# Optimization experiments

Measured on AMD Instinct MI355X. Metric: run time of the kernel, lower is better.

The kernel has to match this reference:

```python
import jax, jax.numpy as jnp
import numpy as np

B, IN, O, F, FH = 512, 2000, 64, 8, 32
D = 64 + FH * O  # 2112


def setup_inputs() -> dict:
    key = jax.random.key(0)
    ks = jax.random.split(key, 17)
    rn = lambda k, s: jax.random.normal(k, s, dtype=jnp.float32) * 0.05
    return dict(
        x=rn(ks[0], (B, IN)),
        fc_in_W=rn(ks[1], (1024, IN)), fc_in_b=rn(ks[2], (1024,)),
        fc1_W=rn(ks[3], (128, 1024)), fc1_b=rn(ks[4], (128,)),
        out1_W=rn(ks[5], (O, 64, 128)), out1_b=rn(ks[6], (O, 64)),
        coef_nn_W=rn(ks[7], (F, FH, 1)), coef_nn_b=rn(ks[8], (F, FH)),
        coef_att_W=rn(ks[9], (F, FH, FH)),
        out_att_W=rn(ks[10], (O, FH, FH)),
        nodes_trans_W=rn(ks[11], (O, O)),
        trans_gcn_W=rn(ks[12], (D, D)),
        outmap_W=rn(ks[13], (1, D)), outmap_b=rn(ks[14], (1,)),
        prelu_a=jnp.float32(0.25),
        coef_m=rn(ks[15], (O, O, F)),
    )


def reference(x, fc_in_W, fc_in_b, fc1_W, fc1_b, out1_W, out1_b,
              coef_nn_W, coef_nn_b, coef_att_W, out_att_W,
              nodes_trans_W, trans_gcn_W, outmap_W, outmap_b, prelu_a, coef_m):
    elu = jax.nn.elu
    # trunk MLP
    h = jax.nn.relu(x @ fc_in_W.T + fc_in_b)          # [B,1024]
    h = jax.nn.relu(h @ fc1_W.T + fc1_b)              # [B,128]
    # per-output-node heads (vectorized over the output_dim loop)
    hiddens = jax.nn.relu(jnp.einsum('bk,odk->bod', h, out1_W) + out1_b)  # [B,O,64]
    # per-feature coef embedding: Linear(1,FH) on each coef_m[:,:,i] slice
    cf = elu(coef_m[..., None] * coef_nn_W[:, :, 0] + coef_nn_b)          # [O,O,F,FH]
    # sum over concatenated feature axis (F*FH) of exp(elu(.))
    s = jnp.exp(elu(cf)).sum(axis=(2, 3))[:, :, None, None]               # [O,O,1,1]
    lin = jnp.einsum('xyfh,fgh->xyfg', cf, coef_att_W)                    # per-feature attention linear
    p = elu(jnp.exp(elu(cf)) * lin / s)
    cfs = elu(p.sum(axis=2) / F)                                          # [O,O,FH]
    # node-level attention (vectorized over the output_dim loop)
    coef_sum = jnp.exp(elu(cfs)).sum(axis=1)                              # [O,FH]
    p2 = jnp.exp(elu(cfs)) / coef_sum[:, None, :]                         # [O,O,FH]
    lin2 = jnp.einsum('oih,igh->oig', cfs, out_att_W)
    att = (p2 * lin2).reshape(O, O * FH)                                  # concat over i (i-major)
    hc = jnp.concatenate(
        [hiddens, jnp.broadcast_to(att[None], (x.shape[0], O, O * FH))], axis=2)  # [B,O,D]
    nt = jnp.einsum('bpd,op->bod', hc, nodes_trans_W)                     # node mixing Linear(O,O)
    trans = jax.nn.sigmoid(jnp.einsum('bod,ed->boe', nt, trans_gcn_W))    # [B,O,D]
    z = (trans @ outmap_W.T + outmap_b).squeeze(-1)                       # [B,O]
    return jnp.where(z >= 0, z, prelu_a * z)                              # PReLU
```

## Files before the change

### kernel.cpp

```cpp
#include <hip/hip_runtime.h>
#include <math.h>

typedef __attribute__((ext_vector_type(8))) short bf16x8;
typedef __attribute__((ext_vector_type(4))) float f32x4;

static __device__ __forceinline__ float fast_elu(float x) {
    return x > 0.0f ? x : __expf(x) - 1.0f;
}

static __device__ __forceinline__ unsigned short f2bf(float f) {
    unsigned int u = __float_as_uint(f);
    unsigned int r = (u + 0x7FFFu + ((u >> 16) & 1u)) >> 16;
    return (unsigned short)r;
}

static __device__ __forceinline__ bf16x8 cvt8(const float* __restrict__ s) {
    float4 a = *reinterpret_cast<const float4*>(s);
    float4 b = *reinterpret_cast<const float4*>(s + 4);
    bf16x8 r;
    r[0] = (short)f2bf(a.x); r[1] = (short)f2bf(a.y);
    r[2] = (short)f2bf(a.z); r[3] = (short)f2bf(a.w);
    r[4] = (short)f2bf(b.x); r[5] = (short)f2bf(b.y);
    r[6] = (short)f2bf(b.z); r[7] = (short)f2bf(b.w);
    return r;
}

#define S0 131072
#define S1 393216
#define S2 409600
#define S3 410112
#define S4 475648
#define S5 492544
#define CONV_BLOCKS 1924

static __device__ __forceinline__ void conv_phase(
    int bx,
    const float* __restrict__ x, const float* __restrict__ fcinW,
    const float* __restrict__ fc1W, const float* __restrict__ ntW,
    const float* __restrict__ out1W, const float* __restrict__ tgw,
    unsigned short* __restrict__ xb, unsigned short* __restrict__ fcinWb,
    unsigned short* __restrict__ fc1Wb, unsigned short* __restrict__ Wb,
    unsigned short* __restrict__ out1WbT, unsigned short* __restrict__ Gb)
{
    int u = bx * 256 + threadIdx.x;
    if (u < S0) {
        int r = u >> 8, c = u & 255;
        bf16x8 v;
        if (c < 250) v = cvt8(&x[(size_t)r * 2000 + c * 8]);
        else { bf16x8 z = {0,0,0,0,0,0,0,0}; v = z; }
        *reinterpret_cast<bf16x8*>(&xb[(size_t)r * 2048 + c * 8]) = v;
    } else if (u < S1) {
        int i = u - S0;
        int r = i >> 8, c = i & 255;
        bf16x8 v;
        if (c < 250) v = cvt8(&fcinW[(size_t)r * 2000 + c * 8]);
        else { bf16x8 z = {0,0,0,0,0,0,0,0}; v = z; }
        *reinterpret_cast<bf16x8*>(&fcinWb[(size_t)r * 2048 + c * 8]) = v;
    } else if (u < S2) {
        int i8 = (u - S1) * 8;
        *reinterpret_cast<bf16x8*>(&fc1Wb[i8]) = cvt8(&fc1W[i8]);
    } else if (u < S3) {
        int i8 = (u - S2) * 8;
        *reinterpret_cast<bf16x8*>(&Wb[i8]) = cvt8(&ntW[i8]);
    } else if (u < S4) {
        int i = u - S3;
        int n = i >> 4, kc = i & 15;
        int d = n >> 6, p = n & 63;
        *reinterpret_cast<bf16x8*>(&out1WbT[(size_t)n * 128 + kc * 8]) =
            cvt8(&out1W[(size_t)((p << 6) | d) * 128 + kc * 8]);
    } else if (u < S5) {
        int i = u - S4;
        int e = i >> 3, c = i & 7;
        *reinterpret_cast<bf16x8*>(&Gb[(size_t)e * 64 + c * 8]) =
            cvt8(&tgw[(size_t)e * 2112 + c * 8]);
    }
}

static __device__ __forceinline__ void coef_phase(
    int bx, float* __restrict__ smemf,
    const float* __restrict__ coef_m, const float* __restrict__ cW,
    const float* __restrict__ cB, const float* __restrict__ attW,
    float* __restrict__ cfs)
{
    float* cf_s = smemf;
    float* part = smemf + 1024;
    const int t = threadIdx.x;
    const int wv = t >> 6, lane = t & 63;
    const int xy = bx * 4 + wv;
    float ls = 0.0f;
    #pragma unroll
    for (int i = 0; i < 4; ++i) {
        int idx = i * 64 + lane;
        int f = idx >> 5;
        float v = fast_elu(coef_m[xy * 8 + f] * cW[idx] + cB[idx]);
        cf_s[wv * 256 + idx] = v;
        ls += __expf(fast_elu(v));
    }
    #pragma unroll
    for (int m = 1; m < 64; m <<= 1) ls += __shfl_xor(ls, m, 64);
    __syncthreads();
    const float rs = __builtin_amdgcn_rcpf(ls);
    const int g = lane & 31, fg = lane >> 5;
    float acc = 0.0f;
    for (int f = fg * 4; f < fg * 4 + 4; ++f) {
        float lin = 0.0f;
        #pragma unroll
        for (int h = 0; h < 32; h += 4) {
            float4 Lv = *reinterpret_cast<const float4*>(&cf_s[wv * 256 + f * 32 + h]);
            float4 Wv = *reinterpret_cast<const float4*>(&attW[f * 1024 + g * 32 + h]);
            lin += Lv.x * Wv.x + Lv.y * Wv.y + Lv.z * Wv.z + Lv.w * Wv.w;
        }
        float e = __expf(fast_elu(cf_s[wv * 256 + f * 32 + g]));
        acc += fast_elu(e * lin * rs);
    }
    part[wv * 64 + lane] = acc;
    __syncthreads();
    if (lane < 32) {
        float tot = part[wv * 64 + lane] + part[wv * 64 + lane + 32];
        cfs[xy * 32 + lane] = fast_elu(tot * 0.125f);
    }
}

static __device__ __forceinline__ void att_phase(
    int o, int ic, float* __restrict__ smemf,
    const float* __restrict__ cfs, const float* __restrict__ oattW,
    float* __restrict__ att)
{
    float* L    = smemf;
    float* red  = smemf + 2048;
    float* csum = smemf + 2304;
    const int t = threadIdx.x;
    #pragma unroll
    for (int j = 0; j < 8; ++j) L[t + 256 * j] = cfs[o * 2048 + t + 256 * j];
    __syncthreads();
    {
        int h = t & 31, ig = t >> 5;
        float ps = 0.0f;
        for (int i = ig * 8; i < ig * 8 + 8; ++i) ps += __expf(fast_elu(L[i * 32 + h]));
        red[t] = ps;
        __syncthreads();
        if (t < 32) {
            float cs = 0.0f;
            #pragma unroll
            for (int j = 0; j < 8; ++j) cs += red[j * 32 + t];
            csum[t] = cs;
        }
        __syncthreads();
    }
    int idx = ic * 256 + t;
    int i = idx >> 5, g = idx & 31;
    float lin2 = 0.0f;
    #pragma unroll
    for (int h = 0; h < 32; h += 4) {
        float4 Lv = *reinterpret_cast<const float4*>(&L[i * 32 + h]);
        float4 Wv = *reinterpret_cast<const float4*>(&oattW[i * 1024 + g * 32 + h]);
        lin2 += Lv.x * Wv.x + Lv.y * Wv.y + Lv.z * Wv.z + Lv.w * Wv.w;
    }
    float p2 = __expf(fast_elu(L[idx])) * __builtin_amdgcn_rcpf(csum[g]);
    att[o * 2048 + idx] = p2 * lin2;
}

static __device__ __forceinline__ void natt_phase(
    int bx, float* __restrict__ smemf,
    const float* __restrict__ ntW, const float* __restrict__ att,
    unsigned short* __restrict__ nattb)
{
    float* ntW_s = smemf;
    float* att_s = smemf + 64 * 65;
    const int t = threadIdx.x;
    const int d0 = bx * 16;
    #pragma unroll
    for (int j = 0; j < 16; ++j) {
        int idx = t + 256 * j;
        ntW_s[(idx >> 6) * 65 + (idx & 63)] = ntW[idx];
    }
    #pragma unroll
    for (int j = 0; j < 4; ++j) {
        int idx = t + 256 * j;
        int p = idx >> 4, dd = idx & 15;
        att_s[p * 17 + dd] = att[p * 2048 + d0 + dd];
    }
    __syncthreads();
    const int dd = t & 15, ob = (t >> 4) * 4;
    float acc[4] = {0.0f, 0.0f, 0.0f, 0.0f};
    for (int p = 0; p < 64; ++p) {
        float av = att_s[p * 17 + dd];
        #pragma unroll
        for (int i = 0; i < 4; ++i) acc[i] += ntW_s[(ob + i) * 65 + p] * av;
    }
    #pragma unroll
    for (int i = 0; i < 4; ++i)
        nattb[(ob + i) * 2048 + d0 + dd] = f2bf(acc[i]);
}

static __device__ __forceinline__ void gemm_core(
    const unsigned short* __restrict__ A, int lda,
    const unsigned short* __restrict__ B, int ldb,
    float* __restrict__ C, unsigned short* __restrict__ Cb,
    int ldc, long strideCz, const float* __restrict__ bias,
    int mode, int kchunk, int bn, int bm, int bz,
    unsigned short* __restrict__ As, unsigned short* __restrict__ Bs)
{
    const int t = threadIdx.x;
    const int w = t >> 6, lane = t & 63, l16 = lane & 15, quad = lane >> 4;
    const int n0 = bn * 64, m0 = bm * 64;
    const int kb0 = bz * kchunk;
    const int r = t >> 2, koff = (t & 3) * 8;
    if (mode == 0) C += (size_t)bz * strideCz;

    const size_t arow = (size_t)(m0 + r) * lda + koff;
    const size_t brow = (size_t)(n0 + r) * ldb + koff;
    bf16x8 av = *reinterpret_cast<const bf16x8*>(&A[arow + kb0]);
    bf16x8 bv = *reinterpret_cast<const bf16x8*>(&B[brow + kb0]);

    f32x4 acc[4] = {};
    for (int kb = kb0; kb < kb0 + kchunk; kb += 32) {
        __syncthreads();
        *reinterpret_cast<bf16x8*>(&As[r * 40 + koff]) = av;
        *reinterpret_cast<bf16x8*>(&Bs[r * 40 + koff]) = bv;
        if (kb + 32 < kb0 + kchunk) {
            av = *reinterpret_cast<const bf16x8*>(&A[arow + kb + 32]);
            bv = *reinterpret_cast<const bf16x8*>(&B[brow + kb + 32]);
        }
        __syncthreads();
        bf16x8 af = *reinterpret_cast<const bf16x8*>(&As[(w * 16 + l16) * 40 + quad * 8]);
        #pragma unroll
        for (int nt = 0; nt < 4; ++nt) {
            bf16x8 bf = *reinterpret_cast<const bf16x8*>(&Bs[(nt * 16 + l16) * 40 + quad * 8]);
            acc[nt] = __builtin_amdgcn_mfma_f32_16x16x32_bf16(af, bf, acc[nt], 0, 0, 0);
        }
    }
    #pragma unroll
    for (int nt = 0; nt < 4; ++nt)
        #pragma unroll
        for (int i = 0; i < 4; ++i) {
            int m = m0 + w * 16 + quad * 4 + i;
            int n = n0 + nt * 16 + l16;
            if (mode == 0) {
                C[(size_t)m * ldc + n] = acc[nt][i];
            } else {
                int bidx = (((n & 63) << 6) | (n >> 6));
                float v = acc[nt][i] + bias[bidx];
                v = fmaxf(v, 0.0f);
                Cb[(size_t)m * ldc + n] = f2bf(v);
            }
        }
}

static __device__ __forceinline__ void gemm_tgwa_core(
    const float* __restrict__ tgw,
    const unsigned short* __restrict__ B,
    float* __restrict__ C, long strideCz,
    int kchunk, int bm, int bz,
    unsigned short* __restrict__ As, unsigned short* __restrict__ Bs)
{
    const int t = threadIdx.x;
    const int w = t >> 6, lane = t & 63, l16 = lane & 15, quad = lane >> 4;
    const int m0 = bm * 64;
    const int kb0 = bz * kchunk;
    const int r = t >> 2, koff = (t & 3) * 8;
    C += (size_t)bz * strideCz;

    const float* arow = tgw + (size_t)(m0 + r) * 2112 + 64 + koff;
    const unsigned short* brow = B + (size_t)r * 2048 + koff;
    bf16x8 av = cvt8(arow + kb0);
    bf16x8 bv = *reinterpret_cast<const bf16x8*>(brow + kb0);

    f32x4 acc[4] = {};
    for (int kb = kb0; kb < kb0 + kchunk; kb += 32) {
        __syncthreads();
        *reinterpret_cast<bf16x8*>(&As[r * 40 + koff]) = av;
        *reinterpret_cast<bf16x8*>(&Bs[r * 40 + koff]) = bv;
        if (kb + 32 < kb0 + kchunk) {
            av = cvt8(arow + kb + 32);
            bv = *reinterpret_cast<const bf16x8*>(brow + kb + 32);
        }
        __syncthreads();
        bf16x8 af = *reinterpret_cast<const bf16x8*>(&As[(w * 16 + l16) * 40 + quad * 8]);
        #pragma unroll
        for (int nt = 0; nt < 4; ++nt) {
            bf16x8 bf = *reinterpret_cast<const bf16x8*>(&Bs[(nt * 16 + l16) * 40 + quad * 8]);
            acc[nt] = __builtin_amdgcn_mfma_f32_16x16x32_bf16(af, bf, acc[nt], 0, 0, 0);
        }
    }
    #pragma unroll
    for (int nt = 0; nt < 4; ++nt)
        #pragma unroll
        for (int i = 0; i < 4; ++i) {
            int m = m0 + w * 16 + quad * 4 + i;
            int n = nt * 16 + l16;
            C[(size_t)m * 64 + n] = acc[nt][i];
        }
}

static __device__ __forceinline__ void gemm_fa_core(
    const float* __restrict__ Ap, int lda, long apstride, int nparts,
    const float* __restrict__ abias,
    const unsigned short* __restrict__ B, int ldb,
    float* __restrict__ C, unsigned short* __restrict__ Cb,
    int ldc, long strideCz, const float* __restrict__ bias,
    int mode, int kchunk, int bn, int bm, int bz,
    unsigned short* __restrict__ As, unsigned short* __restrict__ Bs)
{
    const int t = threadIdx.x;
    const int w = t >> 6, lane = t & 63, l16 = lane & 15, quad = lane >> 4;
    const int n0 = bn * 64, m0 = bm * 64;
    const int kb0 = bz * kchunk;
    const int r = t >> 2, koff = (t & 3) * 8;
    if (mode == 0) C += (size_t)bz * strideCz;

    f32x4 acc[4] = {};
    for (int kb = kb0; kb < kb0 + kchunk; kb += 32) {
        float a8[8];
        {
            const float* base = &Ap[(size_t)(m0 + r) * lda + kb + koff];
            float4 s0 = *reinterpret_cast<const float4*>(base);
            float4 s1 = *reinterpret_cast<const float4*>(base + 4);
            for (int j = 1; j < nparts; ++j) {
                const float* pj = base + (size_t)j * apstride;
                float4 p0 = *reinterpret_cast<const float4*>(pj);
                float4 p1 = *reinterpret_cast<const float4*>(pj + 4);
                s0.x += p0.x; s0.y += p0.y; s0.z += p0.z; s0.w += p0.w;
                s1.x += p1.x; s1.y += p1.y; s1.z += p1.z; s1.w += p1.w;
            }
            float4 b0 = *reinterpret_cast<const float4*>(&abias[kb + koff]);
            float4 b1 = *reinterpret_cast<const float4*>(&abias[kb + koff + 4]);
            a8[0] = fmaxf(s0.x + b0.x, 0.0f); a8[1] = fmaxf(s0.y + b0.y, 0.0f);
            a8[2] = fmaxf(s0.z + b0.z, 0.0f); a8[3] = fmaxf(s0.w + b0.w, 0.0f);
            a8[4] = fmaxf(s1.x + b1.x, 0.0f); a8[5] = fmaxf(s1.y + b1.y, 0.0f);
            a8[6] = fmaxf(s1.z + b1.z, 0.0f); a8[7] = fmaxf(s1.w + b1.w, 0.0f);
        }
        bf16x8 bv = *reinterpret_cast<const bf16x8*>(&B[(size_t)(n0 + r) * ldb + kb + koff]);
        __syncthreads();
        ushort4 lo, hi;
        lo.x = f2bf(a8[0]); lo.y = f2bf(a8[1]); lo.z = f2bf(a8[2]); lo.w = f2bf(a8[3]);
        hi.x = f2bf(a8[4]); hi.y = f2bf(a8[5]); hi.z = f2bf(a8[6]); hi.w = f2bf(a8[7]);
        *reinterpret_cast<ushort4*>(&As[r * 40 + koff]) = lo;
        *reinterpret_cast<ushort4*>(&As[r * 40 + koff + 4]) = hi;
        *reinterpret_cast<bf16x8*>(&Bs[r * 40 + koff]) = bv;
        __syncthreads();
        bf16x8 af = *reinterpret_cast<const bf16x8*>(&As[(w * 16 + l16) * 40 + quad * 8]);
        #pragma unroll
        for (int nt = 0; nt < 4; ++nt) {
            bf16x8 bf = *reinterpret_cast<const bf16x8*>(&Bs[(nt * 16 + l16) * 40 + quad * 8]);
            acc[nt] = __builtin_amdgcn_mfma_f32_16x16x32_bf16(af, bf, acc[nt], 0, 0, 0);
        }
    }
    #pragma unroll
    for (int nt = 0; nt < 4; ++nt)
        #pragma unroll
        for (int i = 0; i < 4; ++i) {
            int m = m0 + w * 16 + quad * 4 + i;
            int n = n0 + nt * 16 + l16;
            if (mode == 0) {
                C[(size_t)m * ldc + n] = acc[nt][i];
            } else {
                int bidx = (((n & 63) << 6) | (n >> 6));
                float v = acc[nt][i] + bias[bidx];
                v = fmaxf(v, 0.0f);
                Cb[(size_t)m * ldc + n] = f2bf(v);
            }
        }
}

static __device__ __forceinline__ void nt1f_phase(
    int b, unsigned short* __restrict__ smemu,
    const unsigned short* __restrict__ hbT, const unsigned short* __restrict__ Wb,
    unsigned short* __restrict__ nt1b)
{
    unsigned short* HtT   = smemu;
    unsigned short* nt1_s = smemu + 64 * 72;
    const int t = threadIdx.x;
    const int w = t >> 6, lane = t & 63, l16 = lane & 15, quad = lane >> 4;

    const unsigned short* src = hbT + (size_t)b * 4096;
    #pragma unroll
    for (int j = 0; j < 2; ++j) {
        int c = t + j * 256;
        *reinterpret_cast<bf16x8*>(&HtT[(c >> 3) * 72 + (c & 7) * 8]) =
            *reinterpret_cast<const bf16x8*>(&src[c * 8]);
    }
    __syncthreads();

    bf16x8 aW[2];
    #pragma unroll
    for (int h = 0; h < 2; ++h)
        aW[h] = *reinterpret_cast<const bf16x8*>(&Wb[(w * 16 + l16) * 64 + h * 32 + quad * 8]);
    #pragma unroll
    for (int dt = 0; dt < 4; ++dt) {
        f32x4 acc = {0.0f, 0.0f, 0.0f, 0.0f};
        #pragma unroll
        for (int h = 0; h < 2; ++h) {
            bf16x8 bf = *reinterpret_cast<const bf16x8*>(
                &HtT[(dt * 16 + l16) * 72 + h * 32 + quad * 8]);
            acc = __builtin_amdgcn_mfma_f32_16x16x32_bf16(aW[h], bf, acc, 0, 0, 0);
        }
        #pragma unroll
        for (int i = 0; i < 4; ++i)
            nt1_s[(w * 16 + quad * 4 + i) * 72 + dt * 16 + l16] = f2bf(acc[i]);
    }
    __syncthreads();
    #pragma unroll
    for (int j = 0; j < 2; ++j) {
        int c = t + j * 256;
        *reinterpret_cast<bf16x8*>(&nt1b[(size_t)b * 4096 + c * 8]) =
            *reinterpret_cast<const bf16x8*>(&nt1_s[(c >> 3) * 72 + (c & 7) * 8]);
    }
}

__global__ __launch_bounds__(256) void uber1(
    const float* x, const float* fcinW, const float* fc1W, const float* ntW,
    const float* out1W, const float* tgw,
    unsigned short* xb, unsigned short* fcinWb, unsigned short* fc1Wb,
    unsigned short* Wb, unsigned short* out1WbT, unsigned short* Gb,
    const float* coef_m, const float* cW, const float* cB, const float* attW,
    float* cfs)
{
    __shared__ __align__(16) float smemf[1280];
    int bx = blockIdx.x;
    if (bx < CONV_BLOCKS)
        conv_phase(bx, x, fcinW, fc1W, ntW, out1W, tgw,
                   xb, fcinWb, fc1Wb, Wb, out1WbT, Gb);
    else
        coef_phase(bx - CONV_BLOCKS, smemf, coef_m, cW, cB, attW, cfs);
}

__global__ __launch_bounds__(256) void uber2(
    const unsigned short* xb, const unsigned short* fcinWb, float* h1p,
    const float* cfs, const float* oattW, float* att)
{
    __shared__ __align__(16) float smemf[2592];
    int bx = blockIdx.x;
    if (bx < 512) {
        unsigned short* As = (unsigned short*)smemf;
        gemm_core(xb, 2048, fcinWb, 2048, h1p, nullptr, 1024, 524288L,
                  nullptr, 0, 512, bx & 15, (bx >> 4) & 7, bx >> 7, As, As + 2560);
    } else {
        int b2 = bx - 512;
        att_phase(b2 & 63, b2 >> 6, smemf, cfs, oattW, att);
    }
}

__global__ __launch_bounds__(256) void uber3(
    const float* h1p, const float* fc_in_b, const unsigned short* fc1Wb,
    float* h2p,
    const float* ntW, const float* att, unsigned short* nattb)
{
    __shared__ __align__(16) float smemf[5248];
    int bx = blockIdx.x;
    if (bx < 64) {
        unsigned short* As = (unsigned short*)smemf;
        gemm_fa_core(h1p, 1024, 524288L, 4, fc_in_b, fc1Wb, 1024,
                     h2p, nullptr, 128, 65536L, nullptr, 0, 256,
                     bx & 1, (bx >> 1) & 7, bx >> 4, As, As + 2560);
    } else {
        natt_phase(bx - 64, smemf, ntW, att, nattb);
    }
}

__global__ __launch_bounds__(256) void uber4(
    const float* h2p, const float* fc1_b, const unsigned short* out1WbT,
    unsigned short* hbT, const float* out1_b,
    const float* tgw, const unsigned short* nattb, float* cpT)
{
    __shared__ __align__(16) float smemf[2560];
    unsigned short* As = (unsigned short*)smemf;
    int bx = blockIdx.x;
    if (bx < 512) {
        gemm_fa_core(h2p, 128, 65536L, 4, fc1_b, out1WbT, 128,
                     nullptr, hbT, 4096, 0L, out1_b, 2, 128,
                     bx & 63, bx >> 6, 0, As, As + 2560);
    } else {
        int b2 = bx - 512;
        gemm_tgwa_core(tgw, nattb, cpT, 135168L, 256,
                       b2 % 33, b2 / 33, As, As + 2560);
    }
}

__global__ __launch_bounds__(256) void uber5(
    const unsigned short* hbT, const unsigned short* Wb, unsigned short* nt1b,
    const float* cpT, float* cmatT)
{
    __shared__ __align__(16) unsigned short smemu[2 * 64 * 72];
    int bx = blockIdx.x;
    if (bx < 512) {
        nt1f_phase(bx, smemu, hbT, Wb, nt1b);
    } else {
        int i = (bx - 512) * 256 + threadIdx.x;
        if (i < 135168) {
            float a = 0.0f;
            #pragma unroll
            for (int j = 0; j < 8; ++j) a += cpT[i + (long)j * 135168L];
            cmatT[i] = a;
        }
    }
}

__global__ __launch_bounds__(256) void final_nb(
    const unsigned short* __restrict__ nt1b,
    const unsigned short* __restrict__ Gb,
    const float* __restrict__ cmatT,
    const float* __restrict__ outW,
    float* __restrict__ zpart)
{
    const int t = threadIdx.x;
    const int w = t >> 6, lane = t & 63, l16 = lane & 15, quad = lane >> 4;
    const int eb = blockIdx.x;
    const int b0 = blockIdx.y * 16;
    const int o = w * 16 + l16;

    bf16x8 ga[4][2];
    float cm[4][4], wv[4][4];
    #pragma unroll
    for (int et = 0; et < 4; ++et) {
        #pragma unroll
        for (int h = 0; h < 2; ++h)
            ga[et][h] = *reinterpret_cast<const bf16x8*>(
                &Gb[(size_t)(eb * 64 + et * 16 + l16) * 64 + h * 32 + quad * 8]);
        #pragma unroll
        for (int i = 0; i < 4; ++i) {
            int e = eb * 64 + et * 16 + quad * 4 + i;
            cm[et][i] = cmatT[(size_t)e * 64 + o];
            wv[et][i] = outW[e];
        }
    }

    const unsigned short* bbase = nt1b + (size_t)b0 * 4096 + o * 64 + quad * 8;
    bf16x8 bf0 = *reinterpret_cast<const bf16x8*>(bbase);
    bf16x8 bf1 = *reinterpret_cast<const bf16x8*>(bbase + 32);

    for (int bi = 0; bi < 16; ++bi) {
        bf16x8 nb0, nb1;
        if (bi < 15) {
            nb0 = *reinterpret_cast<const bf16x8*>(bbase + (size_t)(bi + 1) * 4096);
            nb1 = *reinterpret_cast<const bf16x8*>(bbase + (size_t)(bi + 1) * 4096 + 32);
        }
        float zo = 0.0f;
        #pragma unroll
        for (int et = 0; et < 4; ++et) {
            f32x4 acc = {cm[et][0], cm[et][1], cm[et][2], cm[et][3]};
            acc = __builtin_amdgcn_mfma_f32_16x16x32_bf16(ga[et][0], bf0, acc, 0, 0, 0);
            acc = __builtin_amdgcn_mfma_f32_16x16x32_bf16(ga[et][1], bf1, acc, 0, 0, 0);
            #pragma unroll
            for (int i = 0; i < 4; ++i)
                zo += __builtin_amdgcn_rcpf(1.0f + __expf(-acc[i])) * wv[et][i];
        }
        zo += __shfl_xor(zo, 16, 64);
        zo += __shfl_xor(zo, 32, 64);
        if (quad == 0)
            zpart[((size_t)eb * 512 + b0 + bi) * 64 + o] = zo;
        bf0 = nb0; bf1 = nb1;
    }
}

__global__ __launch_bounds__(256) void finish_kernel(
    const float* __restrict__ zpart, const float* __restrict__ outB,
    const float* __restrict__ preluA, float* __restrict__ out)
{
    int i = blockIdx.x * 256 + threadIdx.x;
    float z = 0.0f;
    for (int j = 0; j < 33; ++j) z += zpart[(size_t)j * 32768 + i];
    z += outB[0];
    float pa = preluA[0];
    out[i] = (z >= 0.0f) ? z : pa * z;
}

extern "C" void kernel_launch(void* const* d_in, const int* in_sizes, int n_in,
                              void* d_out, int out_size, void* d_ws, size_t ws_size,
                              hipStream_t stream)
{
    const float* x       = (const float*)d_in[0];
    const float* fc_in_W = (const float*)d_in[1];
    const float* fc_in_b = (const float*)d_in[2];
    const float* fc1_W   = (const float*)d_in[3];
    const float* fc1_b   = (const float*)d_in[4];
    const float* out1_W  = (const float*)d_in[5];
    const float* out1_b  = (const float*)d_in[6];
    const float* cW      = (const float*)d_in[7];
    const float* cB      = (const float*)d_in[8];
    const float* cattW   = (const float*)d_in[9];
    const float* oattW   = (const float*)d_in[10];
    const float* ntW     = (const float*)d_in[11];
    const float* tgw     = (const float*)d_in[12];
    const float* outW    = (const float*)d_in[13];
    const float* outB    = (const float*)d_in[14];
    const float* preluA  = (const float*)d_in[15];
    const float* coef_m  = (const float*)d_in[16];
    float* out = (float*)d_out;
    float* ws  = (float*)d_ws;

    unsigned short* xb      = (unsigned short*)(ws + 0);
    unsigned short* fcinWb  = (unsigned short*)(ws + 524288);
    unsigned short* fc1Wb   = (unsigned short*)(ws + 1572864);
    unsigned short* Wb      = (unsigned short*)(ws + 1638400);
    unsigned short* out1WbT = (unsigned short*)(ws + 1640448);
    unsigned short* Gb      = (unsigned short*)(ws + 1902592);
    float*          cfs     = ws + 1970176;
    float*          att     = ws + 2101248;
    unsigned short* nattb   = (unsigned short*)(ws + 2232320);
    float*          h1p     = ws + 2297856;
    float*          h2p     = ws + 4395008;
    unsigned short* hbT     = (unsigned short*)(ws + 4657152);
    float*          cpT     = ws + 5705728;
    float*          cmatT   = ws + 6787072;
    unsigned short* nt1b    = (unsigned short*)(ws + 6922240);
    float*          zpart   = ws + 7970816;

    uber1<<<CONV_BLOCKS + 1024, 256, 0, stream>>>(
        x, fc_in_W, fc1_W, ntW, out1_W, tgw,
        xb, fcinWb, fc1Wb, Wb, out1WbT, Gb,
        coef_m, cW, cB, cattW, cfs);
    uber2<<<1024, 256, 0, stream>>>(xb, fcinWb, h1p, cfs, oattW, att);
    uber3<<<192, 256, 0, stream>>>(h1p, fc_in_b, fc1Wb, h2p, ntW, att, nattb);
    uber4<<<776, 256, 0, stream>>>(h2p, fc1_b, out1WbT, hbT, out1_b,
                                   tgw, nattb, cpT);
    uber5<<<1040, 256, 0, stream>>>(hbT, Wb, nt1b, cpT, cmatT);
    final_nb<<<dim3(33, 32), 256, 0, stream>>>(nt1b, Gb, cmatT, outW, zpart);
    finish_kernel<<<128, 256, 0, stream>>>(zpart, outB, preluA, out);
}
```

Measured before the change: 193.9 us.

## Fuse fp32-to-bf16 conversion of x and fc_in_W into first GEMM, drop split-K

The first-layer GEMM now reads fp32 x and fc_in_W directly and converts them to bf16 while loading its tiles, so the separate conversion pass and its bf16 staging buffers go away. The 4-way split-K over 512 blocks is replaced by 128 full-K blocks that apply bias and ReLU in the epilogue and write bf16 h1. The next GEMM then reads bf16 h1 with the plain core instead of summing fp32 partials. This removes a large round trip through memory and a reduction step, but leaves fewer blocks for the big GEMM, each with a longer K loop and conversion work inside it.

```diff
diff --git a/kernel.cpp b/kernel.cpp
--- a/kernel.cpp
+++ b/kernel.cpp
@@ -25,51 +25,34 @@
     return r;
 }
 
-#define S0 131072
-#define S1 393216
-#define S2 409600
-#define S3 410112
-#define S4 475648
-#define S5 492544
-#define CONV_BLOCKS 1924
+#define T0 16384
+#define T1 16896
+#define T2 82432
+#define T3 99328
+#define CONV_BLOCKS 388
 
 static __device__ __forceinline__ void conv_phase(
     int bx,
-    const float* __restrict__ x, const float* __restrict__ fcinW,
     const float* __restrict__ fc1W, const float* __restrict__ ntW,
     const float* __restrict__ out1W, const float* __restrict__ tgw,
-    unsigned short* __restrict__ xb, unsigned short* __restrict__ fcinWb,
     unsigned short* __restrict__ fc1Wb, unsigned short* __restrict__ Wb,
     unsigned short* __restrict__ out1WbT, unsigned short* __restrict__ Gb)
 {
     int u = bx * 256 + threadIdx.x;
-    if (u < S0) {
-        int r = u >> 8, c = u & 255;
-        bf16x8 v;
-        if (c < 250) v = cvt8(&x[(size_t)r * 2000 + c * 8]);
-        else { bf16x8 z = {0,0,0,0,0,0,0,0}; v = z; }
-        *reinterpret_cast<bf16x8*>(&xb[(size_t)r * 2048 + c * 8]) = v;
-    } else if (u < S1) {
-        int i = u - S0;
-        int r = i >> 8, c = i & 255;
-        bf16x8 v;
-        if (c < 250) v = cvt8(&fcinW[(size_t)r * 2000 + c * 8]);
-        else { bf16x8 z = {0,0,0,0,0,0,0,0}; v = z; }
-        *reinterpret_cast<bf16x8*>(&fcinWb[(size_t)r * 2048 + c * 8]) = v;
-    } else if (u < S2) {
-        int i8 = (u - S1) * 8;
+    if (u < T0) {
+        int i8 = u * 8;
         *reinterpret_cast<bf16x8*>(&fc1Wb[i8]) = cvt8(&fc1W[i8]);
-    } else if (u < S3) {
-        int i8 = (u - S2) * 8;
+    } else if (u < T1) {
+        int i8 = (u - T0) * 8;
         *reinterpret_cast<bf16x8*>(&Wb[i8]) = cvt8(&ntW[i8]);
-    } else if (u < S4) {
-        int i = u - S3;
+    } else if (u < T2) {
+        int i = u - T1;
         int n = i >> 4, kc = i & 15;
         int d = n >> 6, p = n & 63;
         *reinterpret_cast<bf16x8*>(&out1WbT[(size_t)n * 128 + kc * 8]) =
             cvt8(&out1W[(size_t)((p << 6) | d) * 128 + kc * 8]);
-    } else if (u < S5) {
-        int i = u - S4;
+    } else if (u < T3) {
+        int i = u - T2;
         int e = i >> 3, c = i & 7;
         *reinterpret_cast<bf16x8*>(&Gb[(size_t)e * 64 + c * 8]) =
             cvt8(&tgw[(size_t)e * 2112 + c * 8]);
@@ -196,9 +179,8 @@
 static __device__ __forceinline__ void gemm_core(
     const unsigned short* __restrict__ A, int lda,
     const unsigned short* __restrict__ B, int ldb,
-    float* __restrict__ C, unsigned short* __restrict__ Cb,
-    int ldc, long strideCz, const float* __restrict__ bias,
-    int mode, int kchunk, int bn, int bm, int bz,
+    float* __restrict__ C, int ldc, long strideCz,
+    int kchunk, int bn, int bm, int bz,
     unsigned short* __restrict__ As, unsigned short* __restrict__ Bs)
 {
     const int t = threadIdx.x;
@@ -206,7 +188,7 @@
     const int n0 = bn * 64, m0 = bm * 64;
     const int kb0 = bz * kchunk;
     const int r = t >> 2, koff = (t & 3) * 8;
-    if (mode == 0) C += (size_t)bz * strideCz;
+    C += (size_t)bz * strideCz;
 
     const size_t arow = (size_t)(m0 + r) * lda + koff;
     const size_t brow = (size_t)(n0 + r) * ldb + koff;
@@ -236,14 +218,55 @@
         for (int i = 0; i < 4; ++i) {
             int m = m0 + w * 16 + quad * 4 + i;
             int n = n0 + nt * 16 + l16;
-            if (mode == 0) {
-                C[(size_t)m * ldc + n] = acc[nt][i];
-            } else {
-                int bidx = (((n & 63) << 6) | (n >> 6));
-                float v = acc[nt][i] + bias[bidx];
-                v = fmaxf(v, 0.0f);
-                Cb[(size_t)m * ldc + n] = f2bf(v);
-            }
+            C[(size_t)m * ldc + n] = acc[nt][i];
+        }
+}
+
+static __device__ __forceinline__ void gemm_xf_core(
+    const float* __restrict__ A, const float* __restrict__ B,
+    const float* __restrict__ bias, unsigned short* __restrict__ Cb,
+    int bn, int bm,
+    unsigned short* __restrict__ As, unsigned short* __restrict__ Bs)
+{
+    const int t = threadIdx.x;
+    const int w = t >> 6, lane = t & 63, l16 = lane & 15, quad = lane >> 4;
+    const int n0 = bn * 64, m0 = bm * 64;
+    const int r = t >> 2, koff = (t & 3) * 8;
+
+    const float* arow = A + (size_t)(m0 + r) * 2000;
+    const float* brow = B + (size_t)(n0 + r) * 2000;
+    const bf16x8 zv = {0, 0, 0, 0, 0, 0, 0, 0};
+
+    bf16x8 av = (koff < 2000) ? cvt8(arow + koff) : zv;
+    bf16x8 bv = (koff < 2000) ? cvt8(brow + koff) : zv;
+
+    f32x4 acc[4] = {};
+    for (int kb = 0; kb < 2000; kb += 32) {
+        __syncthreads();
+        *reinterpret_cast<bf16x8*>(&As[r * 40 + koff]) = av;
+        *reinterpret_cast<bf16x8*>(&Bs[r * 40 + koff]) = bv;
+        if (kb + 32 < 2000) {
+            int k = kb + 32 + koff;
+            av = (k < 2000) ? cvt8(arow + k) : zv;
+            bv = (k < 2000) ? cvt8(brow + k) : zv;
+        }
+        __syncthreads();
+        bf16x8 af = *reinterpret_cast<const bf16x8*>(&As[(w * 16 + l16) * 40 + quad * 8]);
+        #pragma unroll
+        for (int nt = 0; nt < 4; ++nt) {
+            bf16x8 bf = *reinterpret_cast<const bf16x8*>(&Bs[(nt * 16 + l16) * 40 + quad * 8]);
+            acc[nt] = __builtin_amdgcn_mfma_f32_16x16x32_bf16(af, bf, acc[nt], 0, 0, 0);
+        }
+    }
+    #pragma unroll
+    for (int nt = 0; nt < 4; ++nt)
+        #pragma unroll
+        for (int i = 0; i < 4; ++i) {
+            int m = m0 + w * 16 + quad * 4 + i;
+            int n = n0 + nt * 16 + l16;
+            float v = acc[nt][i] + bias[n];
+            v = fmaxf(v, 0.0f);
+            Cb[(size_t)m * 1024 + n] = f2bf(v);
         }
 }
 
@@ -297,20 +320,18 @@
     const float* __restrict__ Ap, int lda, long apstride, int nparts,
     const float* __restrict__ abias,
     const unsigned short* __restrict__ B, int ldb,
-    float* __restrict__ C, unsigned short* __restrict__ Cb,
-    int ldc, long strideCz, const float* __restrict__ bias,
-    int mode, int kchunk, int bn, int bm, int bz,
+    unsigned short* __restrict__ Cb, int ldc,
+    const float* __restrict__ bias,
+    int kchunk, int bn, int bm,
     unsigned short* __restrict__ As, unsigned short* __restrict__ Bs)
 {
     const int t = threadIdx.x;
     const int w = t >> 6, lane = t & 63, l16 = lane & 15, quad = lane >> 4;
     const int n0 = bn * 64, m0 = bm * 64;
-    const int kb0 = bz * kchunk;
     const int r = t >> 2, koff = (t & 3) * 8;
-    if (mode == 0) C += (size_t)bz * strideCz;
 
     f32x4 acc[4] = {};
-    for (int kb = kb0; kb < kb0 + kchunk; kb += 32) {
+    for (int kb = 0; kb < kchunk; kb += 32) {
         float a8[8];
         {
             const float* base = &Ap[(size_t)(m0 + r) * lda + kb + koff];
@@ -352,14 +373,10 @@
         for (int i = 0; i < 4; ++i) {
             int m = m0 + w * 16 + quad * 4 + i;
             int n = n0 + nt * 16 + l16;
-            if (mode == 0) {
-                C[(size_t)m * ldc + n] = acc[nt][i];
-            } else {
-                int bidx = (((n & 63) << 6) | (n >> 6));
-                float v = acc[nt][i] + bias[bidx];
-                v = fmaxf(v, 0.0f);
-                Cb[(size_t)m * ldc + n] = f2bf(v);
-            }
+            int bidx = (((n & 63) << 6) | (n >> 6));
+            float v = acc[nt][i] + bias[bidx];
+            v = fmaxf(v, 0.0f);
+            Cb[(size_t)m * ldc + n] = f2bf(v);
         }
 }
 
@@ -409,50 +426,46 @@
 }
 
 __global__ __launch_bounds__(256) void uber1(
-    const float* x, const float* fcinW, const float* fc1W, const float* ntW,
-    const float* out1W, const float* tgw,
-    unsigned short* xb, unsigned short* fcinWb, unsigned short* fc1Wb,
-    unsigned short* Wb, unsigned short* out1WbT, unsigned short* Gb,
+    const float* fc1W, const float* ntW, const float* out1W, const float* tgw,
+    unsigned short* fc1Wb, unsigned short* Wb, unsigned short* out1WbT,
+    unsigned short* Gb,
     const float* coef_m, const float* cW, const float* cB, const float* attW,
     float* cfs)
 {
     __shared__ __align__(16) float smemf[1280];
     int bx = blockIdx.x;
     if (bx < CONV_BLOCKS)
-        conv_phase(bx, x, fcinW, fc1W, ntW, out1W, tgw,
-                   xb, fcinWb, fc1Wb, Wb, out1WbT, Gb);
+        conv_phase(bx, fc1W, ntW, out1W, tgw, fc1Wb, Wb, out1WbT, Gb);
     else
         coef_phase(bx - CONV_BLOCKS, smemf, coef_m, cW, cB, attW, cfs);
 }
 
 __global__ __launch_bounds__(256) void uber2(
-    const unsigned short* xb, const unsigned short* fcinWb, float* h1p,
+    const float* x, const float* fcinW, const float* fc_in_b,
+    unsigned short* h1b,
     const float* cfs, const float* oattW, float* att)
 {
     __shared__ __align__(16) float smemf[2592];
     int bx = blockIdx.x;
-    if (bx < 512) {
+    if (bx < 128) {
         unsigned short* As = (unsigned short*)smemf;
-        gemm_core(xb, 2048, fcinWb, 2048, h1p, nullptr, 1024, 524288L,
-                  nullptr, 0, 512, bx & 15, (bx >> 4) & 7, bx >> 7, As, As + 2560);
+        gemm_xf_core(x, fcinW, fc_in_b, h1b, bx & 15, bx >> 4, As, As + 2560);
     } else {
-        int b2 = bx - 512;
+        int b2 = bx - 128;
         att_phase(b2 & 63, b2 >> 6, smemf, cfs, oattW, att);
     }
 }
 
 __global__ __launch_bounds__(256) void uber3(
-    const float* h1p, const float* fc_in_b, const unsigned short* fc1Wb,
-    float* h2p,
+    const unsigned short* h1b, const unsigned short* fc1Wb, float* h2p,
     const float* ntW, const float* att, unsigned short* nattb)
 {
     __shared__ __align__(16) float smemf[5248];
     int bx = blockIdx.x;
     if (bx < 64) {
         unsigned short* As = (unsigned short*)smemf;
-        gemm_fa_core(h1p, 1024, 524288L, 4, fc_in_b, fc1Wb, 1024,
-                     h2p, nullptr, 128, 65536L, nullptr, 0, 256,
-                     bx & 1, (bx >> 1) & 7, bx >> 4, As, As + 2560);
+        gemm_core(h1b, 1024, fc1Wb, 1024, h2p, 128, 65536L,
+                  256, bx & 1, (bx >> 1) & 7, bx >> 4, As, As + 2560);
     } else {
         natt_phase(bx - 64, smemf, ntW, att, nattb);
     }
@@ -468,8 +481,7 @@
     int bx = blockIdx.x;
     if (bx < 512) {
         gemm_fa_core(h2p, 128, 65536L, 4, fc1_b, out1WbT, 128,
-                     nullptr, hbT, 4096, 0L, out1_b, 2, 128,
-                     bx & 63, bx >> 6, 0, As, As + 2560);
+                     hbT, 4096, out1_b, 128, bx & 63, bx >> 6, As, As + 2560);
     } else {
         int b2 = bx - 512;
         gemm_tgwa_core(tgw, nattb, cpT, 135168L, 256,
@@ -589,29 +601,26 @@
     float* out = (float*)d_out;
     float* ws  = (float*)d_ws;
 
-    unsigned short* xb      = (unsigned short*)(ws + 0);
-    unsigned short* fcinWb  = (unsigned short*)(ws + 524288);
-    unsigned short* fc1Wb   = (unsigned short*)(ws + 1572864);
-    unsigned short* Wb      = (unsigned short*)(ws + 1638400);
-    unsigned short* out1WbT = (unsigned short*)(ws + 1640448);
-    unsigned short* Gb      = (unsigned short*)(ws + 1902592);
-    float*          cfs     = ws + 1970176;
-    float*          att     = ws + 2101248;
-    unsigned short* nattb   = (unsigned short*)(ws + 2232320);
-    float*          h1p     = ws + 2297856;
-    float*          h2p     = ws + 4395008;
-    unsigned short* hbT     = (unsigned short*)(ws + 4657152);
-    float*          cpT     = ws + 5705728;
-    float*          cmatT   = ws + 6787072;
-    unsigned short* nt1b    = (unsigned short*)(ws + 6922240);
-    float*          zpart   = ws + 7970816;
+    unsigned short* fc1Wb   = (unsigned short*)(ws + 0);
+    unsigned short* Wb      = (unsigned short*)(ws + 65536);
+    unsigned short* out1WbT = (unsigned short*)(ws + 67584);
+    unsigned short* Gb      = (unsigned short*)(ws + 329728);
+    float*          cfs     = ws + 397312;
+    float*          att     = ws + 528384;
+    unsigned short* nattb   = (unsigned short*)(ws + 659456);
+    unsigned short* h1b     = (unsigned short*)(ws + 724992);
+    float*          h2p     = ws + 987136;
+    unsigned short* hbT     = (unsigned short*)(ws + 1249280);
+    float*          cpT     = ws + 2297856;
+    float*          cmatT   = ws + 3379200;
+    unsigned short* nt1b    = (unsigned short*)(ws + 3514368);
+    float*          zpart   = ws + 4562944;
 
     uber1<<<CONV_BLOCKS + 1024, 256, 0, stream>>>(
-        x, fc_in_W, fc1_W, ntW, out1_W, tgw,
-        xb, fcinWb, fc1Wb, Wb, out1WbT, Gb,
+        fc1_W, ntW, out1_W, tgw, fc1Wb, Wb, out1WbT, Gb,
         coef_m, cW, cB, cattW, cfs);
-    uber2<<<1024, 256, 0, stream>>>(xb, fcinWb, h1p, cfs, oattW, att);
-    uber3<<<192, 256, 0, stream>>>(h1p, fc_in_b, fc1Wb, h2p, ntW, att, nattb);
+    uber2<<<640, 256, 0, stream>>>(x, fc_in_W, fc_in_b, h1b, cfs, oattW, att);
+    uber3<<<192, 256, 0, stream>>>(h1b, fc1Wb, h2p, ntW, att, nattb);
     uber4<<<776, 256, 0, stream>>>(h2p, fc1_b, out1WbT, hbT, out1_b,
                                    tgw, nattb, cpT);
     uber5<<<1040, 256, 0, stream>>>(hbT, Wb, nt1b, cpT, cmatT);
```

Measured after the change: 234.2 us. +20.7%, slower.
